# Optimization experiments

Measured on AMD Instinct MI355X. Metric: run time of the kernel, lower is better.

## Reference

```python
import jax, jax.numpy as jnp
import numpy as np

B, N_NODE, E_PER, C, HID, HEADS, IN, NL = 16, 1024, 8192, 16, 128, 4, 32, 2
N = B * N_NODE
NEG_SLOPE = 0.2


def setup_inputs() -> dict:
    key = jax.random.key(0)
    ks = jax.random.split(key, 16)
    obs = jax.random.normal(ks[0], (N, IN), jnp.float32)
    # per-graph random edges, guaranteed no self-loops (GATv2Conv re-adds them once)
    src_l = jax.random.randint(ks[1], (B, E_PER), 0, N_NODE)
    off = jax.random.randint(ks[2], (B, E_PER), 1, N_NODE)
    dst_l = (src_l + off) % N_NODE
    base = (jnp.arange(B) * N_NODE)[:, None]
    edge_index = jnp.stack([(src_l + base).reshape(-1), (dst_l + base).reshape(-1)]).astype(jnp.int32)

    def lin(k, fi, fo):
        return (jax.random.normal(k, (fi, fo), jnp.float32) / np.sqrt(fi)).astype(jnp.float32)

    def gat(k):
        sk = jax.random.split(k, 3)
        return {
            'Wl': (jax.random.normal(sk[0], (NL, HID, HEADS * HID), jnp.float32) / np.sqrt(HID)),
            'bl': jnp.zeros((NL, HEADS * HID), jnp.float32),
            'Wr': (jax.random.normal(sk[1], (NL, HID, HEADS * HID), jnp.float32) / np.sqrt(HID)),
            'br': jnp.zeros((NL, HEADS * HID), jnp.float32),
            'att': (jax.random.normal(sk[2], (NL, HEADS, HID), jnp.float32) / np.sqrt(HID)),
            'bias': jnp.zeros((NL, HID), jnp.float32),
            'g': jnp.ones((NL, HID), jnp.float32),
            'beta': jnp.zeros((NL, HID), jnp.float32),
        }

    inp = {'obs': obs, 'edge_index': edge_index, 'n_node': N_NODE,
           'emb_W': lin(ks[3], IN, HID), 'emb_b': jnp.zeros((HID,), jnp.float32),
           'pool_W': lin(ks[4], HID, C), 'pool_b': jnp.zeros((C,), jnp.float32),
           'mlp_W1': lin(ks[5], HID, 4 * HID), 'mlp_b1': jnp.zeros((4 * HID,), jnp.float32),
           'mlp_W2': lin(ks[6], 4 * HID, HID), 'mlp_b2': jnp.zeros((HID,), jnp.float32)}
    for nm, d in (('low', gat(ks[7])), ('high', gat(ks[8]))):
        for k2, v in d.items():
            inp[nm + '_' + k2] = v
    return inp


def _layer_norm(x, g, b):
    mu = x.mean(-1, keepdims=True)
    v = jnp.mean((x - mu) ** 2, -1, keepdims=True)
    return (x - mu) / jnp.sqrt(v + 1e-5) * g + b


def _gatv2(x, src, dst, Wl, bl, Wr, br, att, bias):
    # GATv2Conv: heads H, concat=False (mean over heads), eval mode (no dropout)
    n = x.shape[0]
    H, D = att.shape
    xl = (x @ Wl + bl).reshape(n, H, D)  # source transform (lin_l)
    xr = (x @ Wr + br).reshape(n, H, D)  # target transform (lin_r)
    e = jax.nn.leaky_relu(xl[src] + xr[dst], NEG_SLOPE)  # [E,H,D]
    logit = jnp.einsum('ehd,hd->eh', e, att)
    m = jax.ops.segment_max(logit, dst, num_segments=n)
    p = jnp.exp(logit - m[dst])
    z = jax.ops.segment_sum(p, dst, num_segments=n)
    alpha = p / z[dst]
    out = jax.ops.segment_sum(alpha[:, :, None] * xl[src], dst, num_segments=n)
    return out.mean(axis=1) + bias


def _gat_stack(h, src, dst, Wl, bl, Wr, br, att, bias, g, beta):
    h_res = h
    nl = Wl.shape[0]
    for j in range(nl):
        h_in = h
        h = _gatv2(h, src, dst, Wl[j], bl[j], Wr[j], br[j], att[j], bias[j])
        h = _layer_norm(h, g[j], beta[j])
        if j != nl - 1:
            h = jax.nn.silu(h)
        h = h + h_in  # use_res=True
    return h + h_res


def _forward(obs, edge_index, n_node, emb_W, emb_b, pool_W, pool_b, mlp_W1, mlp_b1, mlp_W2, mlp_b2,
             low_Wl, low_bl, low_Wr, low_br, low_att, low_bias, low_g, low_beta,
             high_Wl, high_bl, high_Wr, high_br, high_att, high_bias, high_g, high_beta):
    n = obs.shape[0]
    h = obs @ emb_W + emb_b
    hh = h
    # low-level edges + self-loops (GATv2Conv add_self_loops; input has none)
    loops = jnp.arange(n, dtype=edge_index.dtype)
    src = jnp.concatenate([edge_index[0], loops])
    dst = jnp.concatenate([edge_index[1], loops])
    h = _gat_stack(h, src, dst, low_Wl, low_bl, low_Wr, low_br, low_att, low_bias, low_g, low_beta)
    # soft pooling
    pooling = jax.nn.softmax(h @ pool_W + pool_b, axis=-1)  # dim=1 == last dim on 2D
    b = n // n_node
    c = pooling.shape[-1]
    s = pooling.reshape(b, n_node, c)
    count = jnp.maximum(s.sum(axis=1), 1e-5)  # sT @ ones, clamp_min(1e-5)
    Hf = jnp.einsum('bnc,bnd->bcd', s, h.reshape(b, n_node, -1)) / count[:, :, None]
    Hf = Hf.reshape(b * c, -1)
    # high-level: fully connected per-graph cluster edges (self-loops already present once)
    hr = jnp.repeat(jnp.arange(c, dtype=jnp.int32), c)
    hc = jnp.tile(jnp.arange(c, dtype=jnp.int32), c)
    offb = (jnp.arange(b, dtype=jnp.int32) * c)[:, None]
    hsrc = (hr[None, :] + offb).reshape(-1)
    hdst = (hc[None, :] + offb).reshape(-1)
    Hf = _gat_stack(Hf, hsrc, hdst, high_Wl, high_bl, high_Wr, high_br, high_att, high_bias, high_g, high_beta)
    # unpool + residual MLP (BaseMLP flat=True: hidden=4*HID, Tanh, residual)
    l_H = jnp.einsum('bnc,bcd->bnd', s, Hf.reshape(b, c, -1)).reshape(n, -1)
    x = l_H + hh
    return jnp.tanh(x @ mlp_W1 + mlp_b1) @ mlp_W2 + mlp_b2 + x


def reference(obs, edge_index, n_node, emb_W, emb_b, pool_W, pool_b, mlp_W1, mlp_b1, mlp_W2, mlp_b2,
              low_Wl, low_bl, low_Wr, low_br, low_att, low_bias, low_g, low_beta,
              high_Wl, high_bl, high_Wr, high_br, high_att, high_bias, high_g, high_beta):
    return _forward(obs, edge_index, n_node, emb_W, emb_b, pool_W, pool_b, mlp_W1, mlp_b1, mlp_W2, mlp_b2,
                    low_Wl, low_bl, low_Wr, low_br, low_att, low_bias, low_g, low_beta,
                    high_Wl, high_bl, high_Wr, high_br, high_att, high_bias, high_g, high_beta)
```

## Files before the change

### kernel.cpp

```cpp
#include <hip/hip_runtime.h>
#include <math.h>

#define NTOT  16384
#define NNODE 1024

typedef unsigned short u16;
typedef unsigned short u16x8 __attribute__((ext_vector_type(8)));
typedef short s16x8 __attribute__((ext_vector_type(8)));
typedef float f32x4 __attribute__((ext_vector_type(4)));

static __device__ __forceinline__ float b2f(u16 u) {
  return __uint_as_float(((unsigned)u) << 16);
}
static __device__ __forceinline__ u16 f2b(float f) {
  unsigned x = __float_as_uint(f);
  return (u16)((x + 0x7FFFu + ((x >> 16) & 1u)) >> 16);
}

typedef __attribute__((address_space(1))) const void gvoid;
typedef __attribute__((address_space(3))) void lvoid;
static __device__ __forceinline__ void gload16(const void* g, void* lds) {
  __builtin_amdgcn_global_load_lds((gvoid*)g, (lvoid*)lds, 16, 0, 0);
}

__global__ __launch_bounds__(64) void emb_k(const float* __restrict__ obs,
    const float* __restrict__ W, const float* __restrict__ b,
    float* __restrict__ h, float* __restrict__ hh, u16* __restrict__ h_bf)
{
  int n = blockIdx.x, l = threadIdx.x;
  __shared__ float ob[32];
  if (l < 32) ob[l] = obs[n * 32 + l];
  __syncthreads();
  float a0 = b[l], a1 = b[64 + l];
  #pragma unroll
  for (int k = 0; k < 32; ++k) {
    float o = ob[k];
    a0 = fmaf(o, W[k * 128 + l], a0);
    a1 = fmaf(o, W[k * 128 + 64 + l], a1);
  }
  size_t base = (size_t)n * 128;
  h[base + l] = a0;  h[base + 64 + l] = a1;
  hh[base + l] = a0; hh[base + 64 + l] = a1;
  h_bf[base + l] = f2b(a0); h_bf[base + 64 + l] = f2b(a1);
}

__global__ void hist_k(const int* __restrict__ ei, int E0, int* __restrict__ deg)
{
  int i = blockIdx.x * blockDim.x + threadIdx.x;
  int ET = E0 + NTOT;
  if (i < ET) {
    int d = (i < E0) ? ei[E0 + i] : (i - E0);
    atomicAdd(&deg[d], 1);
  }
}

__global__ __launch_bounds__(256) void scan_k(const int* __restrict__ deg,
    int* __restrict__ off, int* __restrict__ cursor)
{
  int t = threadIdx.x, lane = t & 63, wid = t >> 6;
  int base = t * 64;
  int sum = 0;
  for (int i = 0; i < 64; ++i) sum += deg[base + i];
  int inc = sum;
  #pragma unroll
  for (int d = 1; d < 64; d <<= 1) {
    int u = __shfl_up(inc, d);
    if (lane >= d) inc += u;
  }
  __shared__ int wt[4];
  if (lane == 63) wt[wid] = inc;
  __syncthreads();
  int woff = 0;
  for (int i = 0; i < wid; ++i) woff += wt[i];
  int run = woff + inc - sum;
  for (int i = 0; i < 64; ++i) {
    off[base + i] = run; cursor[base + i] = run;
    run += deg[base + i];
  }
  if (t == 255) off[NTOT] = run;
}

__global__ void scat_k(const int* __restrict__ ei, int E0,
    int* __restrict__ cursor, int* __restrict__ csr_src)
{
  int i = blockIdx.x * blockDim.x + threadIdx.x;
  int ET = E0 + NTOT;
  if (i < ET) {
    int s, d;
    if (i < E0) { s = ei[i]; d = ei[E0 + i]; } else { s = d = i - E0; }
    int pos = atomicAdd(&cursor[d], 1);
    csr_src[pos] = s;
  }
}

__global__ void wqall_k(const float* __restrict__ lWl, const float* __restrict__ lWr,
                        const float* __restrict__ hWl, const float* __restrict__ hWr,
                        const float* __restrict__ W1, const float* __restrict__ W2,
                        u16* __restrict__ out)
{
  int idx = blockIdx.x * 256 + threadIdx.x;
  if (idx >= 655360) return;
  float v;
  if (idx < 524288) {
    const float* Wl = idx < 262144 ? lWl : hWl;
    const float* Wr = idx < 262144 ? lWr : hWr;
    int r2 = idx & 262143;
    int m = r2 >> 17, r = r2 & 131071;
    int n = r >> 7, k = r & 127;
    const float* W = (n < 512) ? Wl : Wr;
    v = W[(size_t)m * 65536 + (size_t)k * 512 + (n & 511)];
  } else if (idx < 589824) {
    int i = idx - 524288;
    int n = i >> 7, k = i & 127;
    v = W1[k * 512 + n];
  } else {
    int i = idx - 589824;
    int n = i >> 9, k = i & 511;
    v = W2[k * 128 + n];
  }
  out[idx] = f2b(v);
}

__global__ __launch_bounds__(256) void gemm_bf16(
    const u16* __restrict__ A, const u16* __restrict__ Bt,
    const float* __restrict__ bias0, const float* __restrict__ bias1,
    float* __restrict__ Cf, u16* __restrict__ Cb0, u16* __restrict__ Cb1,
    const float* __restrict__ res,
    int M, int K, int N, int Nsplit, int act)
{
  __shared__ u16 Al[128][128];
  __shared__ u16 Bl[128][128];
  const int tid = threadIdx.x;
  const int bm = blockIdx.x * 128, bn = blockIdx.y * 128;
  const int w = tid >> 6, l = tid & 63;
  const int fr = l & 15;
  const int kg = l >> 4;
  const int lrow = l >> 4, gsl = l & 15;

  f32x4 acc[2][8];
  #pragma unroll
  for (int a = 0; a < 2; ++a)
    #pragma unroll
    for (int b = 0; b < 8; ++b)
      acc[a][b] = (f32x4){0.f, 0.f, 0.f, 0.f};

  for (int k0 = 0; k0 < K; k0 += 128) {
    __syncthreads();
    #pragma unroll
    for (int j = 0; j < 8; ++j) {
      int row = w * 32 + j * 4 + lrow;
      int gsrc = gsl ^ (row & 7);
      gload16(A + (size_t)(bm + row) * K + k0 + gsrc * 8, &Al[w * 32 + j * 4][0]);
    }
    #pragma unroll
    for (int j = 0; j < 8; ++j) {
      int row = w * 32 + j * 4 + lrow;
      int gsrc = gsl ^ (row & 7);
      gload16(Bt + (size_t)(bn + row) * K + k0 + gsrc * 8, &Bl[w * 32 + j * 4][0]);
    }
    __syncthreads();
    #pragma unroll
    for (int ks = 0; ks < 4; ++ks) {
      const int g = (ks << 2) + kg;
      const int ar0 = w * 32 + fr, ar1 = ar0 + 16;
      s16x8 a0 = *(const s16x8*)&Al[ar0][(g ^ (ar0 & 7)) << 3];
      s16x8 a1 = *(const s16x8*)&Al[ar1][(g ^ (ar1 & 7)) << 3];
      #pragma unroll
      for (int nr = 0; nr < 8; ++nr) {
        const int br = nr * 16 + fr;
        s16x8 bb = *(const s16x8*)&Bl[br][(g ^ (br & 7)) << 3];
        acc[0][nr] = __builtin_amdgcn_mfma_f32_16x16x32_bf16(a0, bb, acc[0][nr], 0, 0, 0);
        acc[1][nr] = __builtin_amdgcn_mfma_f32_16x16x32_bf16(a1, bb, acc[1][nr], 0, 0, 0);
      }
    }
  }

  #pragma unroll
  for (int mr = 0; mr < 2; ++mr) {
    const int row0 = bm + w * 32 + mr * 16 + (kg << 2);
    #pragma unroll
    for (int nr = 0; nr < 8; ++nr) {
      const int col = bn + nr * 16 + fr;
      const int half = (col >= Nsplit);
      const int c2 = half ? col - Nsplit : col;
      const int str = half ? (N - Nsplit) : Nsplit;
      const float bb = half ? bias1[c2] : bias0[c2];
      u16* cb = half ? Cb1 : Cb0;
      #pragma unroll
      for (int j = 0; j < 4; ++j) {
        float v = acc[mr][nr][j] + bb;
        if (act) v = tanhf(v);
        size_t o = (size_t)(row0 + j) * str + c2;
        if (res) v += res[o];
        if (Cf) Cf[o] = v;
        if (cb) cb[o] = f2b(v);
      }
    }
  }
}

__global__ __launch_bounds__(256) void gemm64_bf16(
    const u16* __restrict__ A, const u16* __restrict__ Bt,
    const float* __restrict__ bias0, const float* __restrict__ bias1,
    float* __restrict__ Cf, u16* __restrict__ Cb0, u16* __restrict__ Cb1,
    const float* __restrict__ res,
    int M, int K, int N, int Nsplit, int act)
{
  __shared__ u16 Al[64][128];
  __shared__ u16 Bl[128][128];
  const int tid = threadIdx.x;
  const int bm = blockIdx.x * 64, bn = blockIdx.y * 128;
  const int w = tid >> 6, l = tid & 63;
  const int fr = l & 15;
  const int kg = l >> 4;
  const int lrow = l >> 4, gsl = l & 15;

  f32x4 acc[8];
  #pragma unroll
  for (int b = 0; b < 8; ++b) acc[b] = (f32x4){0.f, 0.f, 0.f, 0.f};

  for (int k0 = 0; k0 < K; k0 += 128) {
    __syncthreads();
    #pragma unroll
    for (int j = 0; j < 4; ++j) {
      int row = w * 16 + j * 4 + lrow;
      int gsrc = gsl ^ (row & 7);
      gload16(A + (size_t)(bm + row) * K + k0 + gsrc * 8, &Al[w * 16 + j * 4][0]);
    }
    #pragma unroll
    for (int j = 0; j < 8; ++j) {
      int row = w * 32 + j * 4 + lrow;
      int gsrc = gsl ^ (row & 7);
      gload16(Bt + (size_t)(bn + row) * K + k0 + gsrc * 8, &Bl[w * 32 + j * 4][0]);
    }
    __syncthreads();
    #pragma unroll
    for (int ks = 0; ks < 4; ++ks) {
      const int g = (ks << 2) + kg;
      const int ar0 = w * 16 + fr;
      s16x8 a0 = *(const s16x8*)&Al[ar0][(g ^ (ar0 & 7)) << 3];
      #pragma unroll
      for (int nr = 0; nr < 8; ++nr) {
        const int br = nr * 16 + fr;
        s16x8 bb = *(const s16x8*)&Bl[br][(g ^ (br & 7)) << 3];
        acc[nr] = __builtin_amdgcn_mfma_f32_16x16x32_bf16(a0, bb, acc[nr], 0, 0, 0);
      }
    }
  }

  const int row0 = bm + w * 16 + (kg << 2);
  #pragma unroll
  for (int nr = 0; nr < 8; ++nr) {
    const int col = bn + nr * 16 + fr;
    const int half = (col >= Nsplit);
    const int c2 = half ? col - Nsplit : col;
    const int str = half ? (N - Nsplit) : Nsplit;
    const float bb = half ? bias1[c2] : bias0[c2];
    u16* cb = half ? Cb1 : Cb0;
    #pragma unroll
    for (int j = 0; j < 4; ++j) {
      float v = acc[nr][j] + bb;
      if (act) v = tanhf(v);
      size_t o = (size_t)(row0 + j) * str + c2;
      if (res) v += res[o];
      if (Cf) Cf[o] = v;
      if (cb) cb[o] = f2b(v);
    }
  }
}

static __device__ __forceinline__ void estep(
    u16x8 vv, bool valid, u16x8 xrb, const float* attr,
    float& m, float& z, float* acc)
{
  float xv[8], part = 0.f;
  #pragma unroll
  for (int i = 0; i < 8; ++i) {
    xv[i] = b2f(vv[i]);
    float v = xv[i] + b2f(xrb[i]);
    part = fmaf(fmaxf(v, 0.2f * v), attr[i], part);
  }
  part += __shfl_xor(part, 1); part += __shfl_xor(part, 2);
  part += __shfl_xor(part, 4); part += __shfl_xor(part, 8);
  if (!valid) part = -1e30f;
  float mn = fmaxf(m, part);
  float sc = __expf(m - mn);
  float p  = __expf(part - mn);
  z = z * sc + p;
  #pragma unroll
  for (int i = 0; i < 8; ++i) acc[i] = fmaf(acc[i], sc, p * xv[i]);
  m = mn;
}

__global__ __launch_bounds__(64, 4) void gat_agg4(
    const u16* __restrict__ xl, const u16* __restrict__ xr,
    const int* __restrict__ off, const int* __restrict__ srcs,
    const float* __restrict__ att, const float* __restrict__ bias,
    const float* __restrict__ g, const float* __restrict__ beta,
    float* __restrict__ h, u16* __restrict__ h_bf,
    const float* __restrict__ res2, int do_silu, int swz)
{
  int b = blockIdx.x, l = threadIdx.x;
  int dst0;
  if (swz) {
    int xcd = b & 7, i = b >> 3;
    dst0 = (((xcd << 1) + (i >> 8)) << 10) | ((i & 255) << 2);
  } else dst0 = b << 2;

  float attr[8];
  {
    const float4 a0 = *(const float4*)(att + l * 8);
    const float4 a1 = *(const float4*)(att + l * 8 + 4);
    attr[0] = a0.x; attr[1] = a0.y; attr[2] = a0.z; attr[3] = a0.w;
    attr[4] = a1.x; attr[5] = a1.y; attr[6] = a1.z; attr[7] = a1.w;
  }
  u16x8 xrb[4];
  #pragma unroll
  for (int q = 0; q < 4; ++q)
    xrb[q] = *(const u16x8*)(xr + (size_t)(dst0 + q) * 512 + l * 8);

  int sE[4], nE[4];
  #pragma unroll
  for (int q = 0; q < 4; ++q) { sE[q] = off[dst0 + q]; nE[q] = off[dst0 + q + 1] - sE[q]; }
  int nmax = nE[0] > nE[1] ? nE[0] : nE[1];
  nmax = nmax > nE[2] ? nmax : nE[2];
  nmax = nmax > nE[3] ? nmax : nE[3];

  u16x8 v[4]; int ni[4];
  #pragma unroll
  for (int q = 0; q < 4; ++q) {
    v[q] = *(const u16x8*)(xl + (size_t)srcs[sE[q]] * 512 + l * 8);
    ni[q] = (nE[q] > 1) ? srcs[sE[q] + 1] : 0;
  }
  float m[4] = {-1e30f, -1e30f, -1e30f, -1e30f};
  float z[4] = {0.f, 0.f, 0.f, 0.f};
  float acc[4][8] = {};

  for (int e = 0; e < nmax; ++e) {
    u16x8 c0 = v[0], c1 = v[1], c2 = v[2], c3 = v[3];
    if (e + 1 < nmax) {
      #pragma unroll
      for (int q = 0; q < 4; ++q)
        v[q] = *(const u16x8*)(xl + (size_t)ni[q] * 512 + l * 8);
      #pragma unroll
      for (int q = 0; q < 4; ++q)
        if (e + 2 < nE[q]) ni[q] = srcs[sE[q] + e + 2];
    }
    estep(c0, e < nE[0], xrb[0], attr, m[0], z[0], acc[0]);
    estep(c1, e < nE[1], xrb[1], attr, m[1], z[1], acc[1]);
    estep(c2, e < nE[2], xrb[2], attr, m[2], z[2], acc[2]);
    estep(c3, e < nE[3], xrb[3], attr, m[3], z[3], acc[3]);
  }

  const int d0 = (l & 15) * 8;
  float mu[4], rs[4];
  #pragma unroll
  for (int q = 0; q < 4; ++q) {
    const float inv = 0.25f / z[q];
    #pragma unroll
    for (int i = 0; i < 8; ++i) {
      float x = acc[q][i] * inv;
      x += __shfl_xor(x, 16); x += __shfl_xor(x, 32);
      acc[q][i] = x + bias[d0 + i];
    }
    float sa = 0.f;
    #pragma unroll
    for (int i = 0; i < 8; ++i) sa += acc[q][i];
    sa += __shfl_xor(sa, 1); sa += __shfl_xor(sa, 2);
    sa += __shfl_xor(sa, 4); sa += __shfl_xor(sa, 8);
    mu[q] = sa * (1.f / 128.f);
    float va = 0.f;
    #pragma unroll
    for (int i = 0; i < 8; ++i) { float d = acc[q][i] - mu[q]; va += d * d; }
    va += __shfl_xor(va, 1); va += __shfl_xor(va, 2);
    va += __shfl_xor(va, 4); va += __shfl_xor(va, 8);
    rs[q] = rsqrtf(va * (1.f / 128.f) + 1e-5f);
  }
  float oo[8];
  #pragma unroll
  for (int i = 0; i < 8; ++i)
    oo[i] = (l < 32) ? (l < 16 ? acc[0][i] : acc[1][i])
                     : (l < 48 ? acc[2][i] : acc[3][i]);
  const float mmu = (l < 32) ? (l < 16 ? mu[0] : mu[1]) : (l < 48 ? mu[2] : mu[3]);
  const float mrs = (l < 32) ? (l < 16 ? rs[0] : rs[1]) : (l < 48 ? rs[2] : rs[3]);
  const int dd = dst0 + (l >> 4);
  size_t base = (size_t)dd * 128 + d0;
  float4 r0 = *(const float4*)(h + base);
  float4 r1 = *(const float4*)(h + base + 4);
  float rr[8] = {r0.x, r0.y, r0.z, r0.w, r1.x, r1.y, r1.z, r1.w};
  if (res2) {
    float4 q0 = *(const float4*)(res2 + base);
    float4 q1 = *(const float4*)(res2 + base + 4);
    rr[0] += q0.x; rr[1] += q0.y; rr[2] += q0.z; rr[3] += q0.w;
    rr[4] += q1.x; rr[5] += q1.y; rr[6] += q1.z; rr[7] += q1.w;
  }
  float out[8];
  u16x8 hb;
  #pragma unroll
  for (int i = 0; i < 8; ++i) {
    float y = (oo[i] - mmu) * mrs * g[d0 + i] + beta[d0 + i];
    if (do_silu) y = y / (1.f + __expf(-y));
    out[i] = y + rr[i];
    hb[i] = f2b(out[i]);
  }
  *(float4*)(h + base) = make_float4(out[0], out[1], out[2], out[3]);
  *(float4*)(h + base + 4) = make_float4(out[4], out[5], out[6], out[7]);
  *(u16x8*)(h_bf + base) = hb;
}

__global__ __launch_bounds__(64) void gat_fc16(
    const u16* __restrict__ xl, const u16* __restrict__ xr,
    const float* __restrict__ att, const float* __restrict__ bias,
    const float* __restrict__ g, const float* __restrict__ beta,
    float* __restrict__ h, u16* __restrict__ h_bf,
    const float* __restrict__ res2, int do_silu)
{
  int b = blockIdx.x, l = threadIdx.x;
  const int dst0 = b << 2;
  const int gbase = dst0 & ~15;

  float attr[8];
  {
    const float4 a0 = *(const float4*)(att + l * 8);
    const float4 a1 = *(const float4*)(att + l * 8 + 4);
    attr[0] = a0.x; attr[1] = a0.y; attr[2] = a0.z; attr[3] = a0.w;
    attr[4] = a1.x; attr[5] = a1.y; attr[6] = a1.z; attr[7] = a1.w;
  }
  u16x8 xrb[4];
  #pragma unroll
  for (int q = 0; q < 4; ++q)
    xrb[q] = *(const u16x8*)(xr + (size_t)(dst0 + q) * 512 + l * 8);

  float m[4] = {-1e30f, -1e30f, -1e30f, -1e30f};
  float z[4] = {0.f, 0.f, 0.f, 0.f};
  float acc[4][8] = {};
  u16x8 vcur = *(const u16x8*)(xl + (size_t)gbase * 512 + l * 8);
  for (int e = 0; e < 16; ++e) {
    u16x8 c = vcur;
    if (e < 15) vcur = *(const u16x8*)(xl + (size_t)(gbase + e + 1) * 512 + l * 8);
    estep(c, true, xrb[0], attr, m[0], z[0], acc[0]);
    estep(c, true, xrb[1], attr, m[1], z[1], acc[1]);
    estep(c, true, xrb[2], attr, m[2], z[2], acc[2]);
    estep(c, true, xrb[3], attr, m[3], z[3], acc[3]);
  }

  const int d0 = (l & 15) * 8;
  float mu[4], rs[4];
  #pragma unroll
  for (int q = 0; q < 4; ++q) {
    const float inv = 0.25f / z[q];
    #pragma unroll
    for (int i = 0; i < 8; ++i) {
      float x = acc[q][i] * inv;
      x += __shfl_xor(x, 16); x += __shfl_xor(x, 32);
      acc[q][i] = x + bias[d0 + i];
    }
    float sa = 0.f;
    #pragma unroll
    for (int i = 0; i < 8; ++i) sa += acc[q][i];
    sa += __shfl_xor(sa, 1); sa += __shfl_xor(sa, 2);
    sa += __shfl_xor(sa, 4); sa += __shfl_xor(sa, 8);
    mu[q] = sa * (1.f / 128.f);
    float va = 0.f;
    #pragma unroll
    for (int i = 0; i < 8; ++i) { float d = acc[q][i] - mu[q]; va += d * d; }
    va += __shfl_xor(va, 1); va += __shfl_xor(va, 2);
    va += __shfl_xor(va, 4); va += __shfl_xor(va, 8);
    rs[q] = rsqrtf(va * (1.f / 128.f) + 1e-5f);
  }
  float oo[8];
  #pragma unroll
  for (int i = 0; i < 8; ++i)
    oo[i] = (l < 32) ? (l < 16 ? acc[0][i] : acc[1][i])
                     : (l < 48 ? acc[2][i] : acc[3][i]);
  const float mmu = (l < 32) ? (l < 16 ? mu[0] : mu[1]) : (l < 48 ? mu[2] : mu[3]);
  const float mrs = (l < 32) ? (l < 16 ? rs[0] : rs[1]) : (l < 48 ? rs[2] : rs[3]);
  const int dd = dst0 + (l >> 4);
  size_t base = (size_t)dd * 128 + d0;
  float4 r0 = *(const float4*)(h + base);
  float4 r1 = *(const float4*)(h + base + 4);
  float rr[8] = {r0.x, r0.y, r0.z, r0.w, r1.x, r1.y, r1.z, r1.w};
  if (res2) {
    float4 q0 = *(const float4*)(res2 + base);
    float4 q1 = *(const float4*)(res2 + base + 4);
    rr[0] += q0.x; rr[1] += q0.y; rr[2] += q0.z; rr[3] += q0.w;
    rr[4] += q1.x; rr[5] += q1.y; rr[6] += q1.z; rr[7] += q1.w;
  }
  float out[8];
  u16x8 hb;
  #pragma unroll
  for (int i = 0; i < 8; ++i) {
    float y = (oo[i] - mmu) * mrs * g[d0 + i] + beta[d0 + i];
    if (do_silu) y = y / (1.f + __expf(-y));
    out[i] = y + rr[i];
    hb[i] = f2b(out[i]);
  }
  *(float4*)(h + base) = make_float4(out[0], out[1], out[2], out[3]);
  *(float4*)(h + base + 4) = make_float4(out[4], out[5], out[6], out[7]);
  *(u16x8*)(h_bf + base) = hb;
}

#define HF_CHUNK 32
#define HF_NCH   32
__global__ __launch_bounds__(256) void poolhf_k(const float* __restrict__ h,
    const float* __restrict__ pW, const float* __restrict__ pb,
    float* __restrict__ s, float* __restrict__ part, float* __restrict__ cpart)
{
  __shared__ float hs[HF_CHUNK][128];
  __shared__ float Ws[128][16];
  __shared__ float ss[HF_CHUNK][16];
  int b = blockIdx.x >> 5, chunk = blockIdx.x & 31;
  int n0 = b * NNODE + chunk * HF_CHUNK;
  int t = threadIdx.x;
  #pragma unroll
  for (int i = 0; i < 4; ++i) {
    int idx = t + 256 * i;
    int row = idx >> 5, c4 = (idx & 31) * 4;
    *(float4*)&hs[row][c4] = *(const float4*)(h + (size_t)(n0 + row) * 128 + c4);
  }
  #pragma unroll
  for (int i = 0; i < 2; ++i) {
    int idx = t + 256 * i;
    *(float4*)&Ws[idx >> 2][(idx & 3) * 4] = *(const float4*)(pW + idx * 4);
  }
  __syncthreads();
  const int c = t & 15, nA = t >> 4;
  const float bb = pb[c];
  #pragma unroll
  for (int half = 0; half < 2; ++half) {
    const int nn = nA + half * 16;
    float a = bb;
    for (int k = 0; k < 128; ++k) a = fmaf(hs[nn][k], Ws[k][c], a);
    float mx = a;
    mx = fmaxf(mx, __shfl_xor(mx, 1)); mx = fmaxf(mx, __shfl_xor(mx, 2));
    mx = fmaxf(mx, __shfl_xor(mx, 4)); mx = fmaxf(mx, __shfl_xor(mx, 8));
    float p = __expf(a - mx), sum = p;
    sum += __shfl_xor(sum, 1); sum += __shfl_xor(sum, 2);
    sum += __shfl_xor(sum, 4); sum += __shfl_xor(sum, 8);
    float sv = p / sum;
    ss[nn][c] = sv;
    s[(size_t)(n0 + nn) * 16 + c] = sv;
  }
  __syncthreads();
  const int d = t & 127, cg = (t >> 7) * 8;
  float acc[8] = {};
  for (int n = 0; n < HF_CHUNK; ++n) {
    float hv = hs[n][d];
    #pragma unroll
    for (int i = 0; i < 8; ++i) acc[i] = fmaf(ss[n][cg + i], hv, acc[i]);
  }
  float* po = part + (size_t)chunk * 32768 + (size_t)(b * 16 + cg) * 128 + d;
  #pragma unroll
  for (int i = 0; i < 8; ++i) po[i * 128] = acc[i];
  if (t < 16) {
    float cs = 0.f;
    #pragma unroll
    for (int n = 0; n < HF_CHUNK; ++n) cs += ss[n][t];
    cpart[chunk * 256 + b * 16 + t] = cs;
  }
}

__global__ __launch_bounds__(256) void hfr_k(const float* __restrict__ part,
    const float* __restrict__ cpart, float* __restrict__ Hf,
    float* __restrict__ HfRes, u16* __restrict__ Hf_bf)
{
  int o = blockIdx.x * 256 + threadIdx.x;
  int bc = o >> 7;
  float a = 0.f, cnt = 0.f;
  #pragma unroll 8
  for (int ch = 0; ch < HF_NCH; ++ch) {
    a += part[(size_t)ch * 32768 + o];
    cnt += cpart[ch * 256 + bc];
  }
  float v = a / fmaxf(cnt, 1e-5f);
  Hf[o] = v; HfRes[o] = v; Hf_bf[o] = f2b(v);
}

__global__ __launch_bounds__(64) void unpool_k(const float* __restrict__ s,
    const float* __restrict__ Hf, const float* __restrict__ hh,
    float* __restrict__ x, u16* __restrict__ x_bf)
{
  int n = blockIdx.x, l = threadIdx.x;
  int b = n >> 10;
  float a0 = 0.f, a1 = 0.f;
  #pragma unroll
  for (int c = 0; c < 16; ++c) {
    float sv = s[(size_t)n * 16 + c];
    const float* hp = Hf + (size_t)((b << 4) + c) * 128;
    a0 = fmaf(sv, hp[l], a0);
    a1 = fmaf(sv, hp[64 + l], a1);
  }
  size_t base = (size_t)n * 128;
  float v0 = a0 + hh[base + l], v1 = a1 + hh[base + 64 + l];
  x[base + l] = v0; x[base + 64 + l] = v1;
  x_bf[base + l] = f2b(v0); x_bf[base + 64 + l] = f2b(v1);
}

extern "C" void kernel_launch(void* const* d_in, const int* in_sizes, int n_in,
                              void* d_out, int out_size, void* d_ws, size_t ws_size,
                              hipStream_t stream) {
  (void)n_in; (void)out_size; (void)ws_size;
  const float* obs    = (const float*)d_in[0];
  const int*   ei     = (const int*)d_in[1];
  const float* emb_W  = (const float*)d_in[3];
  const float* emb_b  = (const float*)d_in[4];
  const float* pool_W = (const float*)d_in[5];
  const float* pool_b = (const float*)d_in[6];
  const float* mlp_W1 = (const float*)d_in[7];
  const float* mlp_b1 = (const float*)d_in[8];
  const float* mlp_W2 = (const float*)d_in[9];
  const float* mlp_b2 = (const float*)d_in[10];
  const float* lWl = (const float*)d_in[11]; const float* lbl = (const float*)d_in[12];
  const float* lWr = (const float*)d_in[13]; const float* lbr = (const float*)d_in[14];
  const float* latt = (const float*)d_in[15]; const float* lbias = (const float*)d_in[16];
  const float* lg = (const float*)d_in[17]; const float* lbeta = (const float*)d_in[18];
  const float* hWl = (const float*)d_in[19]; const float* hbl = (const float*)d_in[20];
  const float* hWr = (const float*)d_in[21]; const float* hbr = (const float*)d_in[22];
  const float* hatt = (const float*)d_in[23]; const float* hbias = (const float*)d_in[24];
  const float* hg = (const float*)d_in[25]; const float* hbeta = (const float*)d_in[26];

  const int E0 = in_sizes[1] / 2;
  const int ET = E0 + NTOT;

  char* p = (char*)d_ws;
  auto alloc = [&](size_t bytes) -> void* {
    void* q = (void*)p;
    p += (bytes + 255) & ~(size_t)255;
    return q;
  };
  float* h      = (float*)alloc((size_t)NTOT * 128 * 4);
  float* hh     = (float*)alloc((size_t)NTOT * 128 * 4);
  u16*   h_bf   = (u16*)alloc((size_t)NTOT * 128 * 2);
  u16*   xl_bf  = (u16*)alloc((size_t)NTOT * 512 * 2);
  u16*   xr_bf  = (u16*)alloc((size_t)NTOT * 512 * 2);
  u16*   x_bf   = (u16*)alloc((size_t)NTOT * 128 * 2);
  float* s      = (float*)alloc((size_t)NTOT * 16 * 4);
  float* Hf     = (float*)alloc(256 * 128 * 4);
  float* HfRes  = (float*)alloc(256 * 128 * 4);
  u16*   Hf_bf  = (u16*)alloc(256 * 128 * 2);
  u16*   hxl    = (u16*)alloc(256 * 512 * 2);
  u16*   hxr    = (u16*)alloc(256 * 512 * 2);
  float* hfPart = (float*)alloc((size_t)HF_NCH * 32768 * 4);
  float* hfCnt  = (float*)alloc((size_t)HF_NCH * 256 * 4);
  u16*   WT     = (u16*)alloc((size_t)655360 * 2);
  int* deg      = (int*)alloc((size_t)NTOT * 4);
  int* off      = (int*)alloc((size_t)(NTOT + 1) * 4);
  int* cursor   = (int*)alloc((size_t)NTOT * 4);
  int* csr      = (int*)alloc((size_t)ET * 4);
  u16* lWT = WT;
  u16* hWT = WT + 262144;
  u16* W1T = WT + 524288;
  u16* W2T = WT + 589824;
  u16* t_bf = xl_bf;

  wqall_k<<<2560, 256, 0, stream>>>(lWl, lWr, hWl, hWr, mlp_W1, mlp_W2, WT);

  hipMemsetAsync(deg, 0, (size_t)NTOT * 4, stream);
  emb_k<<<NTOT, 64, 0, stream>>>(obs, emb_W, emb_b, h, hh, h_bf);
  hist_k<<<(ET + 255) / 256, 256, 0, stream>>>(ei, E0, deg);
  scan_k<<<1, 256, 0, stream>>>(deg, off, cursor);
  scat_k<<<(ET + 255) / 256, 256, 0, stream>>>(ei, E0, cursor, csr);

  for (int j = 0; j < 2; ++j) {
    gemm_bf16<<<dim3(NTOT / 128, 8), 256, 0, stream>>>(h_bf, lWT + j * 131072,
        lbl + j * 512, lbr + j * 512, nullptr, xl_bf, xr_bf, nullptr,
        NTOT, 128, 1024, 512, 0);
    gat_agg4<<<NTOT / 4, 64, 0, stream>>>(xl_bf, xr_bf, off, csr, latt + j * 512,
        lbias + j * 128, lg + j * 128, lbeta + j * 128, h, h_bf,
        j == 1 ? hh : nullptr, j == 0 ? 1 : 0, 1);
  }

  poolhf_k<<<16 * HF_NCH, 256, 0, stream>>>(h, pool_W, pool_b, s, hfPart, hfCnt);
  hfr_k<<<128, 256, 0, stream>>>(hfPart, hfCnt, Hf, HfRes, Hf_bf);

  for (int j = 0; j < 2; ++j) {
    gemm64_bf16<<<dim3(4, 8), 256, 0, stream>>>(Hf_bf, hWT + j * 131072,
        hbl + j * 512, hbr + j * 512, nullptr, hxl, hxr, nullptr,
        256, 128, 1024, 512, 0);
    gat_fc16<<<64, 64, 0, stream>>>(hxl, hxr, hatt + j * 512, hbias + j * 128,
        hg + j * 128, hbeta + j * 128, Hf, Hf_bf,
        j == 1 ? HfRes : nullptr, j == 0 ? 1 : 0);
  }

  float* x = (float*)d_out;
  unpool_k<<<NTOT, 64, 0, stream>>>(s, Hf, hh, x, x_bf);
  gemm_bf16<<<dim3(NTOT / 128, 4), 256, 0, stream>>>(x_bf, W1T, mlp_b1, mlp_b1,
      nullptr, t_bf, nullptr, nullptr, NTOT, 128, 512, 512, 1);
  gemm64_bf16<<<dim3(NTOT / 64, 1), 256, 0, stream>>>(t_bf, W2T, mlp_b2, mlp_b2,
      x, nullptr, nullptr, x, NTOT, 512, 128, 128, 0);
}
```

Before: 404.7 us.

## Sort nodes by degree and aggregate two destinations per wave

Adds a per-graph counting sort of destination nodes by in-degree (capped at 63), producing a permutation. The GAT aggregation kernel now handles two degree-matched destinations per 64-lane wave instead of four arbitrary ones, which cuts idle iterations from degree imbalance and lowers register pressure. The low-level GEMM also gets an XCD-aware row-block swizzle so xl/xr tiles for one graph land on the same XCD as the aggregation blocks that read them. This costs three extra small kernels and a memset, and the epilogue now leaves half the wave idle.

```diff
diff --git a/kernel.cpp b/kernel.cpp
--- a/kernel.cpp
+++ b/kernel.cpp
@@ -90,6 +90,34 @@
     if (i < E0) { s = ei[i]; d = ei[E0 + i]; } else { s = d = i - E0; }
     int pos = atomicAdd(&cursor[d], 1);
     csr_src[pos] = s;
+  }
+}
+
+__global__ void dhist_k(const int* __restrict__ deg, int* __restrict__ dh)
+{
+  int n = blockIdx.x * 256 + threadIdx.x;
+  if (n < NTOT) {
+    int d = deg[n]; d = d < 63 ? d : 63;
+    atomicAdd(&dh[(n >> 10) * 64 + d], 1);
+  }
+}
+__global__ void dscan_k(const int* __restrict__ dh, int* __restrict__ dcur)
+{
+  int g = threadIdx.x;
+  if (g < 16) {
+    int run = 0;
+    for (int d = 0; d < 64; ++d) { dcur[g * 64 + d] = run; run += dh[g * 64 + d]; }
+  }
+}
+__global__ void dscat_k(const int* __restrict__ deg, int* __restrict__ dcur,
+                        int* __restrict__ perm)
+{
+  int n = blockIdx.x * 256 + threadIdx.x;
+  if (n < NTOT) {
+    int gph = n >> 10;
+    int d = deg[n]; d = d < 63 ? d : 63;
+    int pos = atomicAdd(&dcur[gph * 64 + d], 1);
+    perm[gph * 1024 + pos] = n;
   }
 }
 
@@ -126,12 +154,14 @@
     const float* __restrict__ bias0, const float* __restrict__ bias1,
     float* __restrict__ Cf, u16* __restrict__ Cb0, u16* __restrict__ Cb1,
     const float* __restrict__ res,
-    int M, int K, int N, int Nsplit, int act)
+    int M, int K, int N, int Nsplit, int act, int rswz)
 {
   __shared__ u16 Al[128][128];
   __shared__ u16 Bl[128][128];
   const int tid = threadIdx.x;
-  const int bm = blockIdx.x * 128, bn = blockIdx.y * 128;
+  int bx = blockIdx.x;
+  if (rswz) bx = (bx & 7) * 16 + (bx >> 3);
+  const int bm = bx * 128, bn = blockIdx.y * 128;
   const int w = tid >> 6, l = tid & 63;
   const int fr = l & 15;
   const int kg = l >> 4;
@@ -292,20 +322,22 @@
   m = mn;
 }
 
-__global__ __launch_bounds__(64, 4) void gat_agg4(
+__global__ __launch_bounds__(64) void gat_agg2(
     const u16* __restrict__ xl, const u16* __restrict__ xr,
     const int* __restrict__ off, const int* __restrict__ srcs,
+    const int* __restrict__ perm,
     const float* __restrict__ att, const float* __restrict__ bias,
     const float* __restrict__ g, const float* __restrict__ beta,
     float* __restrict__ h, u16* __restrict__ h_bf,
     const float* __restrict__ res2, int do_silu, int swz)
 {
   int b = blockIdx.x, l = threadIdx.x;
-  int dst0;
+  int slot0;
   if (swz) {
     int xcd = b & 7, i = b >> 3;
-    dst0 = (((xcd << 1) + (i >> 8)) << 10) | ((i & 255) << 2);
-  } else dst0 = b << 2;
+    slot0 = (((xcd << 1) + (i >> 9)) << 10) | ((i & 511) << 1);
+  } else slot0 = b << 1;
+  const int dst0 = perm[slot0], dst1 = perm[slot0 + 1];
 
   float attr[8];
   {
@@ -314,98 +346,94 @@
     attr[0] = a0.x; attr[1] = a0.y; attr[2] = a0.z; attr[3] = a0.w;
     attr[4] = a1.x; attr[5] = a1.y; attr[6] = a1.z; attr[7] = a1.w;
   }
-  u16x8 xrb[4];
-  #pragma unroll
-  for (int q = 0; q < 4; ++q)
-    xrb[q] = *(const u16x8*)(xr + (size_t)(dst0 + q) * 512 + l * 8);
-
-  int sE[4], nE[4];
-  #pragma unroll
-  for (int q = 0; q < 4; ++q) { sE[q] = off[dst0 + q]; nE[q] = off[dst0 + q + 1] - sE[q]; }
-  int nmax = nE[0] > nE[1] ? nE[0] : nE[1];
-  nmax = nmax > nE[2] ? nmax : nE[2];
-  nmax = nmax > nE[3] ? nmax : nE[3];
-
-  u16x8 v[4]; int ni[4];
-  #pragma unroll
-  for (int q = 0; q < 4; ++q) {
-    v[q] = *(const u16x8*)(xl + (size_t)srcs[sE[q]] * 512 + l * 8);
-    ni[q] = (nE[q] > 1) ? srcs[sE[q] + 1] : 0;
-  }
-  float m[4] = {-1e30f, -1e30f, -1e30f, -1e30f};
-  float z[4] = {0.f, 0.f, 0.f, 0.f};
-  float acc[4][8] = {};
+  u16x8 xrb0 = *(const u16x8*)(xr + (size_t)dst0 * 512 + l * 8);
+  u16x8 xrb1 = *(const u16x8*)(xr + (size_t)dst1 * 512 + l * 8);
+
+  const int s0 = off[dst0], n0 = off[dst0 + 1] - s0;
+  const int s1 = off[dst1], n1 = off[dst1 + 1] - s1;
+  const int nmax = n0 > n1 ? n0 : n1;
+
+  int ni0 = (n0 > 1) ? srcs[s0 + 1] : 0;
+  int ni1 = (n1 > 1) ? srcs[s1 + 1] : 0;
+  u16x8 v0 = *(const u16x8*)(xl + (size_t)srcs[s0] * 512 + l * 8);
+  u16x8 v1 = *(const u16x8*)(xl + (size_t)srcs[s1] * 512 + l * 8);
+
+  float m0 = -1e30f, z0 = 0.f, acc0[8] = {};
+  float m1 = -1e30f, z1 = 0.f, acc1[8] = {};
 
   for (int e = 0; e < nmax; ++e) {
-    u16x8 c0 = v[0], c1 = v[1], c2 = v[2], c3 = v[3];
+    u16x8 c0 = v0, c1 = v1;
     if (e + 1 < nmax) {
-      #pragma unroll
-      for (int q = 0; q < 4; ++q)
-        v[q] = *(const u16x8*)(xl + (size_t)ni[q] * 512 + l * 8);
-      #pragma unroll
-      for (int q = 0; q < 4; ++q)
-        if (e + 2 < nE[q]) ni[q] = srcs[sE[q] + e + 2];
-    }
-    estep(c0, e < nE[0], xrb[0], attr, m[0], z[0], acc[0]);
-    estep(c1, e < nE[1], xrb[1], attr, m[1], z[1], acc[1]);
-    estep(c2, e < nE[2], xrb[2], attr, m[2], z[2], acc[2]);
-    estep(c3, e < nE[3], xrb[3], attr, m[3], z[3], acc[3]);
+      v0 = *(const u16x8*)(xl + (size_t)ni0 * 512 + l * 8);
+      v1 = *(const u16x8*)(xl + (size_t)ni1 * 512 + l * 8);
+      if (e + 2 < n0) ni0 = srcs[s0 + e + 2];
+      if (e + 2 < n1) ni1 = srcs[s1 + e + 2];
+    }
+    estep(c0, e < n0, xrb0, attr, m0, z0, acc0);
+    estep(c1, e < n1, xrb1, attr, m1, z1, acc1);
   }
 
   const int d0 = (l & 15) * 8;
-  float mu[4], rs[4];
-  #pragma unroll
-  for (int q = 0; q < 4; ++q) {
-    const float inv = 0.25f / z[q];
+  float o0[8], o1[8];
+  const float inv0 = 0.25f / z0, inv1 = 0.25f / z1;
+  #pragma unroll
+  for (int i = 0; i < 8; ++i) {
+    float v = acc0[i] * inv0;
+    v += __shfl_xor(v, 16); v += __shfl_xor(v, 32);
+    o0[i] = v + bias[d0 + i];
+    float w2 = acc1[i] * inv1;
+    w2 += __shfl_xor(w2, 16); w2 += __shfl_xor(w2, 32);
+    o1[i] = w2 + bias[d0 + i];
+  }
+  float sa = 0.f, sb = 0.f;
+  #pragma unroll
+  for (int i = 0; i < 8; ++i) { sa += o0[i]; sb += o1[i]; }
+  sa += __shfl_xor(sa, 1); sa += __shfl_xor(sa, 2);
+  sa += __shfl_xor(sa, 4); sa += __shfl_xor(sa, 8);
+  sb += __shfl_xor(sb, 1); sb += __shfl_xor(sb, 2);
+  sb += __shfl_xor(sb, 4); sb += __shfl_xor(sb, 8);
+  const float mu0 = sa * (1.f / 128.f), mu1 = sb * (1.f / 128.f);
+  float va = 0.f, vb = 0.f;
+  #pragma unroll
+  for (int i = 0; i < 8; ++i) {
+    float d = o0[i] - mu0; va += d * d;
+    float e = o1[i] - mu1; vb += e * e;
+  }
+  va += __shfl_xor(va, 1); va += __shfl_xor(va, 2);
+  va += __shfl_xor(va, 4); va += __shfl_xor(va, 8);
+  vb += __shfl_xor(vb, 1); vb += __shfl_xor(vb, 2);
+  vb += __shfl_xor(vb, 4); vb += __shfl_xor(vb, 8);
+  const float rstd0 = rsqrtf(va * (1.f / 128.f) + 1e-5f);
+  const float rstd1 = rsqrtf(vb * (1.f / 128.f) + 1e-5f);
+
+  const float* oo = (l < 16) ? o0 : o1;
+  const float mu = (l < 16) ? mu0 : mu1;
+  const float rstd = (l < 16) ? rstd0 : rstd1;
+  const int dd = (l < 16) ? dst0 : dst1;
+  if (l < 32) {
+    size_t base = (size_t)dd * 128 + d0;
+    float4 r0 = *(const float4*)(h + base);
+    float4 r1 = *(const float4*)(h + base + 4);
+    float rr[8] = {r0.x, r0.y, r0.z, r0.w, r1.x, r1.y, r1.z, r1.w};
+    if (res2) {
+      float4 q0 = *(const float4*)(res2 + base);
+      float4 q1 = *(const float4*)(res2 + base + 4);
+      rr[0] += q0.x; rr[1] += q0.y; rr[2] += q0.z; rr[3] += q0.w;
+      rr[4] += q1.x; rr[5] += q1.y; rr[6] += q1.z; rr[7] += q1.w;
+    }
+    float out[8];
+    u16x8 hb;
     #pragma unroll
     for (int i = 0; i < 8; ++i) {
-      float x = acc[q][i] * inv;
-      x += __shfl_xor(x, 16); x += __shfl_xor(x, 32);
-      acc[q][i] = x + bias[d0 + i];
-    }
-    float sa = 0.f;
-    #pragma unroll
-    for (int i = 0; i < 8; ++i) sa += acc[q][i];
-    sa += __shfl_xor(sa, 1); sa += __shfl_xor(sa, 2);
-    sa += __shfl_xor(sa, 4); sa += __shfl_xor(sa, 8);
-    mu[q] = sa * (1.f / 128.f);
-    float va = 0.f;
-    #pragma unroll
-    for (int i = 0; i < 8; ++i) { float d = acc[q][i] - mu[q]; va += d * d; }
-    va += __shfl_xor(va, 1); va += __shfl_xor(va, 2);
-    va += __shfl_xor(va, 4); va += __shfl_xor(va, 8);
-    rs[q] = rsqrtf(va * (1.f / 128.f) + 1e-5f);
-  }
-  float oo[8];
-  #pragma unroll
-  for (int i = 0; i < 8; ++i)
-    oo[i] = (l < 32) ? (l < 16 ? acc[0][i] : acc[1][i])
-                     : (l < 48 ? acc[2][i] : acc[3][i]);
-  const float mmu = (l < 32) ? (l < 16 ? mu[0] : mu[1]) : (l < 48 ? mu[2] : mu[3]);
-  const float mrs = (l < 32) ? (l < 16 ? rs[0] : rs[1]) : (l < 48 ? rs[2] : rs[3]);
-  const int dd = dst0 + (l >> 4);
-  size_t base = (size_t)dd * 128 + d0;
-  float4 r0 = *(const float4*)(h + base);
-  float4 r1 = *(const float4*)(h + base + 4);
-  float rr[8] = {r0.x, r0.y, r0.z, r0.w, r1.x, r1.y, r1.z, r1.w};
-  if (res2) {
-    float4 q0 = *(const float4*)(res2 + base);
-    float4 q1 = *(const float4*)(res2 + base + 4);
-    rr[0] += q0.x; rr[1] += q0.y; rr[2] += q0.z; rr[3] += q0.w;
-    rr[4] += q1.x; rr[5] += q1.y; rr[6] += q1.z; rr[7] += q1.w;
-  }
-  float out[8];
-  u16x8 hb;
-  #pragma unroll
-  for (int i = 0; i < 8; ++i) {
-    float y = (oo[i] - mmu) * mrs * g[d0 + i] + beta[d0 + i];
-    if (do_silu) y = y / (1.f + __expf(-y));
-    out[i] = y + rr[i];
-    hb[i] = f2b(out[i]);
-  }
-  *(float4*)(h + base) = make_float4(out[0], out[1], out[2], out[3]);
-  *(float4*)(h + base + 4) = make_float4(out[4], out[5], out[6], out[7]);
-  *(u16x8*)(h_bf + base) = hb;
+      float y = (oo[i] - mu) * rstd * g[d0 + i] + beta[d0 + i];
+      if (do_silu) y = y / (1.f + __expf(-y));
+      out[i] = y + rr[i];
+      hb[i] = f2b(out[i]);
+    }
+    *(float4*)(h + base) = make_float4(out[0], out[1], out[2], out[3]);
+    *(float4*)(h + base + 4) = make_float4(out[4], out[5], out[6], out[7]);
+    *(u16x8*)(h_bf + base) = hb;
+  }
 }
 
 __global__ __launch_bounds__(64) void gat_fc16(
@@ -647,6 +675,9 @@
   int* off      = (int*)alloc((size_t)(NTOT + 1) * 4);
   int* cursor   = (int*)alloc((size_t)NTOT * 4);
   int* csr      = (int*)alloc((size_t)ET * 4);
+  int* perm     = (int*)alloc((size_t)NTOT * 4);
+  int* dh       = (int*)alloc(16 * 64 * 4);
+  int* dcur     = (int*)alloc(16 * 64 * 4);
   u16* lWT = WT;
   u16* hWT = WT + 262144;
   u16* W1T = WT + 524288;
@@ -656,17 +687,21 @@
   wqall_k<<<2560, 256, 0, stream>>>(lWl, lWr, hWl, hWr, mlp_W1, mlp_W2, WT);
 
   hipMemsetAsync(deg, 0, (size_t)NTOT * 4, stream);
+  hipMemsetAsync(dh, 0, 16 * 64 * 4, stream);
   emb_k<<<NTOT, 64, 0, stream>>>(obs, emb_W, emb_b, h, hh, h_bf);
   hist_k<<<(ET + 255) / 256, 256, 0, stream>>>(ei, E0, deg);
   scan_k<<<1, 256, 0, stream>>>(deg, off, cursor);
   scat_k<<<(ET + 255) / 256, 256, 0, stream>>>(ei, E0, cursor, csr);
+  dhist_k<<<NTOT / 256, 256, 0, stream>>>(deg, dh);
+  dscan_k<<<1, 64, 0, stream>>>(dh, dcur);
+  dscat_k<<<NTOT / 256, 256, 0, stream>>>(deg, dcur, perm);
 
   for (int j = 0; j < 2; ++j) {
     gemm_bf16<<<dim3(NTOT / 128, 8), 256, 0, stream>>>(h_bf, lWT + j * 131072,
         lbl + j * 512, lbr + j * 512, nullptr, xl_bf, xr_bf, nullptr,
-        NTOT, 128, 1024, 512, 0);
-    gat_agg4<<<NTOT / 4, 64, 0, stream>>>(xl_bf, xr_bf, off, csr, latt + j * 512,
-        lbias + j * 128, lg + j * 128, lbeta + j * 128, h, h_bf,
+        NTOT, 128, 1024, 512, 0, 1);
+    gat_agg2<<<NTOT / 2, 64, 0, stream>>>(xl_bf, xr_bf, off, csr, perm,
+        latt + j * 512, lbias + j * 128, lg + j * 128, lbeta + j * 128, h, h_bf,
         j == 1 ? hh : nullptr, j == 0 ? 1 : 0, 1);
   }
 
@@ -685,7 +720,7 @@
   float* x = (float*)d_out;
   unpool_k<<<NTOT, 64, 0, stream>>>(s, Hf, hh, x, x_bf);
   gemm_bf16<<<dim3(NTOT / 128, 4), 256, 0, stream>>>(x_bf, W1T, mlp_b1, mlp_b1,
-      nullptr, t_bf, nullptr, nullptr, NTOT, 128, 512, 512, 1);
+      nullptr, t_bf, nullptr, nullptr, NTOT, 128, 512, 512, 1, 0);
   gemm64_bf16<<<dim3(NTOT / 64, 1), 256, 0, stream>>>(t_bf, W2T, mlp_b2, mlp_b2,
       x, nullptr, nullptr, x, NTOT, 512, 128, 128, 0);
 }
```

Result: faster. 384.8 us (-4.9%).
